# Kernel tuning notes

Hardware: AMD Instinct MI355X
Metric: run time of the kernel (lower is better)

The kernel has to match this reference:

```python
import jax, jax.numpy as jnp
import numpy as np

N_TOKENS = 4096
HIDDEN = 1024
N_EXPERTS = 8
TOP_K = 2
EXPANDED = 2048


def setup_inputs() -> dict:
    key = jax.random.key(0)
    ks = jax.random.split(key, 4)
    tokens = jax.random.normal(ks[0], (N_TOKENS, HIDDEN), dtype=jnp.float32)
    router_w = jax.random.normal(ks[1], (N_EXPERTS, HIDDEN), dtype=jnp.float32) * (1.0 / np.sqrt(HIDDEN))
    router_b = jnp.zeros((N_EXPERTS,), dtype=jnp.float32)
    w1 = jax.random.normal(ks[2], (N_EXPERTS, HIDDEN, EXPANDED), dtype=jnp.float32) * (1.0 / np.sqrt(HIDDEN))
    b1 = jnp.zeros((N_EXPERTS, EXPANDED), dtype=jnp.float32)
    w2 = jax.random.normal(ks[3], (N_EXPERTS, EXPANDED, HIDDEN), dtype=jnp.float32) * (1.0 / np.sqrt(EXPANDED))
    b2 = jnp.zeros((N_EXPERTS, HIDDEN), dtype=jnp.float32)
    return {"tokens": tokens, "router_w": router_w, "router_b": router_b,
            "w1": w1, "b1": b1, "w2": w2, "b2": b2}


def reference(tokens, router_w, router_b, w1, b1, w2, b2):
    # Router: logits [N, E], top-k scores -> softmax over the k selected experts.
    logits = tokens @ router_w.T + router_b
    top_scores, expert_ids = jax.lax.top_k(logits, TOP_K)      # [N, K]
    probs = jax.nn.softmax(top_scores, axis=-1)                # [N, K]

    # Instead of gathering full per-token weight matrices (as the torch code does),
    # run each expert's dense MLP over all tokens and combine with the per-token
    # routing weight for that expert. Identical math: each token's contribution is
    # sum_k probs[n,k] * MLP_{expert_ids[n,k]}(tokens[n]).
    out = jnp.zeros_like(tokens)
    for e in range(N_EXPERTS):
        h = jax.nn.gelu(tokens @ w1[e] + b1[e], approximate=False)  # [N, EXPANDED]
        o = h @ w2[e] + b2[e]                                       # [N, HIDDEN]
        # Combined routing weight for expert e (top_k indices are distinct).
        gate = jnp.sum(jnp.where(expert_ids == e, probs, 0.0), axis=-1)  # [N]
        out = out + gate[:, None] * o
    return out
```

## Files before the change

### kernel.cpp

```cpp
#include <hip/hip_runtime.h>
#include <hip/hip_bf16.h>

typedef unsigned short u16;
typedef __attribute__((ext_vector_type(8))) short short8;
typedef __attribute__((ext_vector_type(4))) float f32x4;

#define N_TOKENS 4096
#define HIDDEN   1024
#define N_EXP    8
#define EXPAND   2048

#define TOKB_OFF  0ull
#define W1T_OFF   8388608ull
#define OBUF_OFF  8388608ull
#define W2T_OFF   41943040ull
#define H_OFF     75497472ull
#define RLT_OFF   109051904ull
#define RLG_OFF   109084672ull
#define CNT_OFF   109117440ull
#define E01_OFF   109117472ull
#define GATE_OFF  109183008ull
#define ROWS2_OFF 109215776ull

__device__ __forceinline__ u16 f2bf(float f) {
  union { float f; unsigned u; } v; v.f = f;
  unsigned r = v.u + 0x7fffu + ((v.u >> 16) & 1u);
  return (u16)(r >> 16);
}

__device__ __forceinline__ void glds16(const void* g, void* l) {
  __builtin_amdgcn_global_load_lds(
      (const __attribute__((address_space(1))) void*)g,
      (__attribute__((address_space(3))) void*)l, 16, 0, 0);
}

__device__ __forceinline__ float gelu_tanh(float x) {
  float u = x * (0.7978845608f + 0.0356774081f * x * x);
  float t = __expf(-2.0f * fabsf(u));
  float th = (1.0f - t) / (1.0f + t);
  th = (u >= 0.0f) ? th : -th;
  return 0.5f * x * (1.0f + th);
}

__global__ __launch_bounds__(256) void cvt_transpose_k(const float* __restrict__ in,
                                                       u16* __restrict__ out,
                                                       int R, int C) {
  __shared__ float t[32][33];
  int e = blockIdx.z;
  int r0 = blockIdx.y * 32, c0 = blockIdx.x * 32;
  const float* ip = in + (size_t)e * R * C;
  u16* op = out + (size_t)e * R * C;
  int tx = threadIdx.x, ty = threadIdx.y;
  #pragma unroll
  for (int i = 0; i < 4; ++i)
    t[ty + i * 8][tx] = ip[(size_t)(r0 + ty + i * 8) * C + c0 + tx];
  __syncthreads();
  #pragma unroll
  for (int i = 0; i < 4; ++i)
    op[(size_t)(c0 + ty + i * 8) * R + r0 + tx] = f2bf(t[tx][ty + i * 8]);
}

__global__ __launch_bounds__(256) void logits_k(const float* __restrict__ tokens,
                                                const float* __restrict__ rw,
                                                const float* __restrict__ rb,
                                                u16* __restrict__ tokb,
                                                int* __restrict__ e01,
                                                float* __restrict__ gates) {
  __shared__ float rwl[N_EXP * HIDDEN];
  int tid = threadIdx.x;
  for (int i = tid; i < N_EXP * HIDDEN; i += 256) rwl[i] = rw[i];
  __syncthreads();
  int w = tid >> 6, l = tid & 63;
  int t = blockIdx.x * 4 + w;
  const float* tp = tokens + (size_t)t * HIDDEN;
  u16* tb = tokb + (size_t)t * HIDDEN;
  float acc[8] = {0.f,0.f,0.f,0.f,0.f,0.f,0.f,0.f};
  for (int k = l; k < HIDDEN; k += 64) {
    float tv = tp[k];
    tb[k] = f2bf(tv);
    #pragma unroll
    for (int e = 0; e < 8; ++e) acc[e] += tv * rwl[e * HIDDEN + k];
  }
  #pragma unroll
  for (int off = 32; off >= 1; off >>= 1) {
    #pragma unroll
    for (int e = 0; e < 8; ++e) acc[e] += __shfl_xor(acc[e], off);
  }
  if (l == 0) {
    float lg[8];
    #pragma unroll
    for (int e = 0; e < 8; ++e) lg[e] = acc[e] + rb[e];
    int b0 = 0; float v0 = lg[0];
    #pragma unroll
    for (int e = 1; e < 8; ++e) if (lg[e] > v0) { v0 = lg[e]; b0 = e; }
    int b1 = -1; float v1 = -3.4e38f;
    #pragma unroll
    for (int e = 0; e < 8; ++e) {
      if (e == b0) continue;
      if (lg[e] > v1) { v1 = lg[e]; b1 = e; }
    }
    float d = expf(v1 - v0);
    float p1 = d / (1.f + d);
    float p0 = 1.f - p1;
    e01[t * 2] = b0;   e01[t * 2 + 1] = b1;
    gates[t * 2] = p0; gates[t * 2 + 1] = p1;
  }
}

__global__ __launch_bounds__(1024) void order_k(const int* __restrict__ e01,
                                                const float* __restrict__ gates,
                                                int* __restrict__ cnt,
                                                int* __restrict__ rlt,
                                                float* __restrict__ rlg,
                                                int* __restrict__ rows2) {
  __shared__ int slotbuf[2 * N_TOKENS];
  __shared__ int wcnt[16][N_EXP];
  __shared__ int base_run[N_EXP];
  __shared__ int basep[N_EXP];
  int tid = threadIdx.x, w = tid >> 6, l = tid & 63;
  if (tid < N_EXP) base_run[tid] = 0;
  __syncthreads();
  unsigned long long ltmask = (1ull << l) - 1ull;
  #pragma unroll
  for (int c = 0; c < 8; ++c) {
    int i = c * 1024 + tid;
    int ei = e01[i];
    int myrank = 0;
    #pragma unroll
    for (int e = 0; e < N_EXP; ++e) {
      unsigned long long b = __ballot(ei == e);
      if (l == 0) wcnt[w][e] = __popcll(b);
      if (ei == e) myrank = __popcll(b & ltmask);
    }
    __syncthreads();
    if (tid < N_EXP) {
      int e = tid, off = base_run[e];
      #pragma unroll
      for (int ww = 0; ww < 16; ++ww) {
        int v = wcnt[ww][e]; wcnt[ww][e] = off; off += v;
      }
      base_run[e] = off;
    }
    __syncthreads();
    slotbuf[i] = wcnt[w][ei] + myrank;
    __syncthreads();
  }
  if (tid < N_EXP) cnt[tid] = base_run[tid];
  if (tid == 0) {
    int s = 0;
    for (int e = 0; e < N_EXP; ++e) { basep[e] = s; s += base_run[e]; }
  }
  __syncthreads();
  #pragma unroll
  for (int c = 0; c < 8; ++c) {
    int i = c * 1024 + tid;
    int e = e01[i];
    int row = basep[e] + slotbuf[i];
    rlt[row] = i >> 1;
    rlg[row] = gates[i];
    rows2[i] = row;
  }
}


#define STAGE(Ad, Bd, KT) {                                                      \
  _Pragma("unroll") for (int c = 0; c < 4; ++c)                                  \
    glds16(ga[c] + (size_t)(KT) * 64, &Ad[(c * 256 + threadIdx.x) * 8]);         \
  _Pragma("unroll") for (int c = 0; c < 2; ++c)                                  \
    glds16(gb[c] + (size_t)(KT) * 64, &Bd[(c * 256 + threadIdx.x) * 8]);         \
}

#define GEMM_TILE(As, Bs) {                                                      \
  _Pragma("unroll") for (int kk = 0; kk < 2; ++kk) {                             \
    short8 afr[4], bfr[2];                                                       \
    _Pragma("unroll") for (int i = 0; i < 4; ++i)                                \
      afr[i] = *(const short8*)&As[oa[kk][i]];                                   \
    _Pragma("unroll") for (int j = 0; j < 2; ++j)                                \
      bfr[j] = *(const short8*)&Bs[ob[kk][j]];                                   \
    _Pragma("unroll") for (int i = 0; i < 4; ++i)                                \
      _Pragma("unroll") for (int j = 0; j < 2; ++j)                              \
        acc[i][j] = __builtin_amdgcn_mfma_f32_16x16x32_bf16(                     \
            afr[i], bfr[j], acc[i][j], 0, 0, 0);                                 \
  }                                                                              \
}

#define FRAG_OFFSETS {                                                           \
  _Pragma("unroll") for (int kk = 0; kk < 2; ++kk) {                             \
    int cc = kk * 4 + lg;                                                        \
    _Pragma("unroll") for (int i = 0; i < 4; ++i) {                              \
      int Ra = wr * 64 + i * 16 + lr;                                            \
      oa[kk][i] = Ra * 64 + (cc ^ (Ra & 7)) * 8;                                 \
    }                                                                            \
    _Pragma("unroll") for (int j = 0; j < 2; ++j) {                              \
      int Rb = wc * 32 + j * 16 + lr;                                            \
      ob[kk][j] = Rb * 64 + (cc ^ (Rb & 7)) * 8;                                 \
    }                                                                            \
  }                                                                              \
}

__global__ __launch_bounds__(256) void ffn1_k(const u16* __restrict__ tok,
                                              const u16* __restrict__ w1t,
                                              const float* __restrict__ b1,
                                              const int* __restrict__ rlt,
                                              const int* __restrict__ cnt,
                                              u16* __restrict__ h) {
  __shared__ __align__(16) short A0[8192];
  __shared__ __align__(16) short A1[8192];
  __shared__ __align__(16) short B0[4096];
  __shared__ __align__(16) short B1[4096];

  int tid = threadIdx.x, w = tid >> 6, l = tid & 63;
  int wr = w >> 1, wc = w & 1;
  int lr = l & 15, lg = l >> 4;
  int oa[2][4], ob[2][2];
  FRAG_OFFSETS

  int e = blockIdx.x & 7;
  int rnk = blockIdx.x >> 3;
  int estr = gridDim.x >> 3;
  int m0 = 0;
  #pragma unroll
  for (int i = 0; i < 8; ++i) { int ci = cnt[i]; if (i < e) m0 += ci; }
  int ne = cnt[e];
  int mts = (ne + 127) >> 7;
  int NT_e = mts * (EXPAND / 64);

  for (int r = rnk; r < NT_e; r += estr) {
    int mt = r >> 5, nt = r & 31;
    int m0g = m0 + mt * 128;
    int mrem = ne - mt * 128;

    const u16* ga[4]; const u16* gb[2];
    #pragma unroll
    for (int c = 0; c < 4; ++c) {
      int flat = c * 256 + tid, rih = flat >> 3;
      int ch = (flat & 7) ^ (rih & 7);
      int tokid = rlt[m0g + ((rih < mrem) ? rih : 0)];
      ga[c] = tok + (size_t)tokid * HIDDEN + ch * 8;
    }
    #pragma unroll
    for (int c = 0; c < 2; ++c) {
      int flat = c * 256 + tid, rih = flat >> 3;
      int ch = (flat & 7) ^ (rih & 7);
      int nrow = nt * 64 + rih;
      gb[c] = w1t + (size_t)e * (EXPAND * HIDDEN) + (size_t)nrow * HIDDEN + ch * 8;
    }

    f32x4 acc[4][2] = {};
    STAGE(A0, B0, 0)
    __syncthreads();
    #pragma unroll 1
    for (int it = 0; it < 8; ++it) {
      STAGE(A1, B1, 2 * it + 1)
      GEMM_TILE(A0, B0)
      __syncthreads();
      if (it < 7) STAGE(A0, B0, 2 * it + 2)
      GEMM_TILE(A1, B1)
      __syncthreads();
    }

    #pragma unroll
    for (int i = 0; i < 4; ++i) {
      #pragma unroll
      for (int rr = 0; rr < 4; ++rr) {
        int row = wr * 64 + i * 16 + lg * 4 + rr;
        if (row >= mrem) continue;
        size_t hrow = (size_t)(m0g + row) * EXPAND;
        #pragma unroll
        for (int j = 0; j < 2; ++j) {
          int col = nt * 64 + wc * 32 + j * 16 + lr;
          float x = acc[i][j][rr] + b1[e * EXPAND + col];
          h[hrow + col] = f2bf(gelu_tanh(x));
        }
      }
    }
  }
}

__global__ __launch_bounds__(256) void ffn2_k(const u16* __restrict__ h,
                                              const u16* __restrict__ w2t,
                                              const float* __restrict__ b2,
                                              const float* __restrict__ rlg,
                                              const int* __restrict__ cnt,
                                              float* __restrict__ obuf) {
  __shared__ __align__(16) short A0[8192];
  __shared__ __align__(16) short A1[8192];
  __shared__ __align__(16) short B0[4096];
  __shared__ __align__(16) short B1[4096];

  int tid = threadIdx.x, w = tid >> 6, l = tid & 63;
  int wr = w >> 1, wc = w & 1;
  int lr = l & 15, lg = l >> 4;
  int oa[2][4], ob[2][2];
  FRAG_OFFSETS

  int e = blockIdx.x & 7;
  int rnk = blockIdx.x >> 3;
  int estr = gridDim.x >> 3;
  int m0 = 0;
  #pragma unroll
  for (int i = 0; i < 8; ++i) { int ci = cnt[i]; if (i < e) m0 += ci; }
  int ne = cnt[e];
  int mts = (ne + 127) >> 7;
  int NT_e = mts * (HIDDEN / 64);

  for (int r = rnk; r < NT_e; r += estr) {
    int mt = r >> 4, nt = r & 15;
    int m0g = m0 + mt * 128;
    int mrem = ne - mt * 128;

    const u16* ga[4]; const u16* gb[2];
    #pragma unroll
    for (int c = 0; c < 4; ++c) {
      int flat = c * 256 + tid, rih = flat >> 3;
      int ch = (flat & 7) ^ (rih & 7);
      int rowg = m0g + ((rih < mrem) ? rih : 0);
      ga[c] = h + (size_t)rowg * EXPAND + ch * 8;
    }
    #pragma unroll
    for (int c = 0; c < 2; ++c) {
      int flat = c * 256 + tid, rih = flat >> 3;
      int ch = (flat & 7) ^ (rih & 7);
      int nrow = nt * 64 + rih;
      gb[c] = w2t + (size_t)e * (HIDDEN * EXPAND) + (size_t)nrow * EXPAND + ch * 8;
    }

    f32x4 acc[4][2] = {};
    STAGE(A0, B0, 0)
    __syncthreads();
    #pragma unroll 1
    for (int it = 0; it < 16; ++it) {
      STAGE(A1, B1, 2 * it + 1)
      GEMM_TILE(A0, B0)
      __syncthreads();
      if (it < 15) STAGE(A0, B0, 2 * it + 2)
      GEMM_TILE(A1, B1)
      __syncthreads();
    }

    #pragma unroll
    for (int i = 0; i < 4; ++i) {
      #pragma unroll
      for (int rr = 0; rr < 4; ++rr) {
        int row = wr * 64 + i * 16 + lg * 4 + rr;
        if (row >= mrem) continue;
        float gate = rlg[m0g + row];
        size_t orow = (size_t)(m0g + row) * HIDDEN;
        #pragma unroll
        for (int j = 0; j < 2; ++j) {
          int col = nt * 64 + wc * 32 + j * 16 + lr;
          obuf[orow + col] = (acc[i][j][rr] + b2[e * HIDDEN + col]) * gate;
        }
      }
    }
  }
}

__global__ __launch_bounds__(256) void combine_k(const float* __restrict__ obuf,
                                                 const int* __restrict__ rows2,
                                                 float* __restrict__ out) {
  int t = blockIdx.x, c = threadIdx.x;
  int r0 = rows2[t * 2], r1 = rows2[t * 2 + 1];
  float4 a = ((const float4*)obuf)[(size_t)r0 * 256 + c];
  float4 b = ((const float4*)obuf)[(size_t)r1 * 256 + c];
  float4 o;
  o.x = a.x + b.x; o.y = a.y + b.y; o.z = a.z + b.z; o.w = a.w + b.w;
  ((float4*)out)[(size_t)t * 256 + c] = o;
}

extern "C" void kernel_launch(void* const* d_in, const int* in_sizes, int n_in,
                              void* d_out, int out_size, void* d_ws, size_t ws_size,
                              hipStream_t stream) {
  const float* tokens   = (const float*)d_in[0];
  const float* router_w = (const float*)d_in[1];
  const float* router_b = (const float*)d_in[2];
  const float* w1       = (const float*)d_in[3];
  const float* b1       = (const float*)d_in[4];
  const float* w2       = (const float*)d_in[5];
  const float* b2       = (const float*)d_in[6];
  float* out = (float*)d_out;

  char* ws = (char*)d_ws;
  u16*   tokb  = (u16*)(ws + TOKB_OFF);
  u16*   w1t   = (u16*)(ws + W1T_OFF);
  float* obuf  = (float*)(ws + OBUF_OFF);
  u16*   w2t   = (u16*)(ws + W2T_OFF);
  u16*   h     = (u16*)(ws + H_OFF);
  int*   rlt   = (int*)(ws + RLT_OFF);
  float* rlg   = (float*)(ws + RLG_OFF);
  int*   cnt   = (int*)(ws + CNT_OFF);
  int*   e01   = (int*)(ws + E01_OFF);
  float* gates = (float*)(ws + GATE_OFF);
  int*   rows2 = (int*)(ws + ROWS2_OFF);

  cvt_transpose_k<<<dim3(EXPAND / 32, HIDDEN / 32, N_EXP), dim3(32, 8), 0, stream>>>(
      w1, w1t, HIDDEN, EXPAND);
  cvt_transpose_k<<<dim3(HIDDEN / 32, EXPAND / 32, N_EXP), dim3(32, 8), 0, stream>>>(
      w2, w2t, EXPAND, HIDDEN);
  logits_k<<<N_TOKENS / 4, 256, 0, stream>>>(tokens, router_w, router_b, tokb, e01, gates);
  order_k<<<1, 1024, 0, stream>>>(e01, gates, cnt, rlt, rlg, rows2);
  ffn1_k<<<2048, 256, 0, stream>>>(tokb, w1t, b1, rlt, cnt, h);
  ffn2_k<<<2048, 256, 0, stream>>>(h, w2t, b2, rlg, cnt, obuf);
  combine_k<<<N_TOKENS, 256, 0, stream>>>(obuf, rows2, out);
}
```

Baseline: 220.6 us.

## Triple-buffer LDS K-loop with explicit vmcnt waits in both FFN GEMMs

Replaces the double-buffered K loop in both expert GEMM kernels with a three-stage LDS ring that prefetches two K-tiles ahead. Raw s_waitcnt vmcnt(6) waits replace the blanket __syncthreads so one stage's global-to-LDS loads can stay in flight across the barrier. The loop is fully unrolled and sched_barrier pins instruction order, so more memory latency should hide behind the MFMA work. The cost is 50% more LDS per block (72 KB instead of 48 KB), which may reduce occupancy, plus larger code.

```diff
diff --git a/kernel.cpp b/kernel.cpp
--- a/kernel.cpp
+++ b/kernel.cpp
@@ -163,6 +163,9 @@
 }
 
 
+#define VM6  asm volatile("s_waitcnt vmcnt(6)" ::: "memory")
+#define VM0  asm volatile("s_waitcnt vmcnt(0)" ::: "memory")
+
 #define STAGE(Ad, Bd, KT) {                                                      \
   _Pragma("unroll") for (int c = 0; c < 4; ++c)                                  \
     glds16(ga[c] + (size_t)(KT) * 64, &Ad[(c * 256 + threadIdx.x) * 8]);         \
@@ -198,6 +201,22 @@
   }                                                                              \
 }
 
+#define KSTEP(Ac, Bc, As, Bs, KT, NK) {                                          \
+  if ((KT) + 2 < (NK)) STAGE(As, Bs, (KT) + 2)                                   \
+  GEMM_TILE(Ac, Bc)                                                              \
+  if ((KT) + 2 < (NK)) { VM6; }                                                  \
+  else if ((KT) + 1 < (NK)) { VM0; }                                             \
+  __builtin_amdgcn_s_barrier();                                                  \
+  __builtin_amdgcn_sched_barrier(0);                                             \
+}
+
+#define K3(k, NK) KSTEP(A0, B0, A2, B2, (k), NK)                                 \
+                  KSTEP(A1, B1, A0, B0, (k) + 1, NK)                             \
+                  KSTEP(A2, B2, A1, B1, (k) + 2, NK)
+
+#define KPROLOGUE { STAGE(A0, B0, 0) STAGE(A1, B1, 1) VM6;                       \
+  __builtin_amdgcn_s_barrier(); __builtin_amdgcn_sched_barrier(0); }
+
 __global__ __launch_bounds__(256) void ffn1_k(const u16* __restrict__ tok,
                                               const u16* __restrict__ w1t,
                                               const float* __restrict__ b1,
@@ -206,8 +225,10 @@
                                               u16* __restrict__ h) {
   __shared__ __align__(16) short A0[8192];
   __shared__ __align__(16) short A1[8192];
+  __shared__ __align__(16) short A2[8192];
   __shared__ __align__(16) short B0[4096];
   __shared__ __align__(16) short B1[4096];
+  __shared__ __align__(16) short B2[4096];
 
   int tid = threadIdx.x, w = tid >> 6, l = tid & 63;
   int wr = w >> 1, wc = w & 1;
@@ -247,17 +268,9 @@
     }
 
     f32x4 acc[4][2] = {};
-    STAGE(A0, B0, 0)
-    __syncthreads();
-    #pragma unroll 1
-    for (int it = 0; it < 8; ++it) {
-      STAGE(A1, B1, 2 * it + 1)
-      GEMM_TILE(A0, B0)
-      __syncthreads();
-      if (it < 7) STAGE(A0, B0, 2 * it + 2)
-      GEMM_TILE(A1, B1)
-      __syncthreads();
-    }
+    KPROLOGUE
+    K3(0, 16) K3(3, 16) K3(6, 16) K3(9, 16) K3(12, 16)
+    KSTEP(A0, B0, A2, B2, 15, 16)
 
     #pragma unroll
     for (int i = 0; i < 4; ++i) {
@@ -285,8 +298,10 @@
                                               float* __restrict__ obuf) {
   __shared__ __align__(16) short A0[8192];
   __shared__ __align__(16) short A1[8192];
+  __shared__ __align__(16) short A2[8192];
   __shared__ __align__(16) short B0[4096];
   __shared__ __align__(16) short B1[4096];
+  __shared__ __align__(16) short B2[4096];
 
   int tid = threadIdx.x, w = tid >> 6, l = tid & 63;
   int wr = w >> 1, wc = w & 1;
@@ -326,17 +341,11 @@
     }
 
     f32x4 acc[4][2] = {};
-    STAGE(A0, B0, 0)
-    __syncthreads();
-    #pragma unroll 1
-    for (int it = 0; it < 16; ++it) {
-      STAGE(A1, B1, 2 * it + 1)
-      GEMM_TILE(A0, B0)
-      __syncthreads();
-      if (it < 15) STAGE(A0, B0, 2 * it + 2)
-      GEMM_TILE(A1, B1)
-      __syncthreads();
-    }
+    KPROLOGUE
+    K3(0, 32) K3(3, 32) K3(6, 32) K3(9, 32) K3(12, 32)
+    K3(15, 32) K3(18, 32) K3(21, 32) K3(24, 32) K3(27, 32)
+    KSTEP(A0, B0, A2, B2, 30, 32)
+    KSTEP(A1, B1, A0, B0, 31, 32)
 
     #pragma unroll
     for (int i = 0; i < 4; ++i) {
```

Result: no change. 219.4 us (-0.5%).
